# Kernel optimization log

Hardware: AMD Instinct MI355X
Metric: run time of the kernel (lower is better)

## Reference

```python
import jax, jax.numpy as jnp
import numpy as np

N_NODES = 50000
N_EDGES = 600000
IN_DIM = 128
HIDDEN = 128


def setup_inputs() -> dict:
    key = jax.random.key(0)
    k1, k2, k3, k4 = jax.random.split(key, 4)
    x = jax.random.normal(k1, (N_NODES, IN_DIM), dtype=jnp.float32)
    edge_index = jax.random.randint(k2, (2, N_EDGES), 0, N_NODES, dtype=jnp.int64)
    # Glorot-ish init for the two GCN layer weights
    W1 = jax.random.normal(k3, (IN_DIM, HIDDEN), dtype=jnp.float32) / np.sqrt(IN_DIM)
    b1 = jnp.zeros((HIDDEN,), dtype=jnp.float32)
    W2 = jax.random.normal(k4, (HIDDEN, HIDDEN), dtype=jnp.float32) / np.sqrt(HIDDEN)
    b2 = jnp.zeros((HIDDEN,), dtype=jnp.float32)
    return {"x": x, "edge_index": edge_index, "W1": W1, "b1": b1, "W2": W2, "b2": b2}


def _gcn_layer(x, W, b, src, dst, deg_inv_sqrt, n_nodes):
    # GCNConv: out = D^{-1/2} (A + I) D^{-1/2} X W + b, computed edge-wise.
    xw = x @ W                                           # [N, H] dense GEMM
    norm = deg_inv_sqrt[src] * deg_inv_sqrt[dst]         # [E+N]
    msg = xw[src] * norm[:, None]                        # gather + scale, [E+N, H]
    agg = jax.ops.segment_sum(msg, dst, num_segments=n_nodes)  # scatter-add
    return agg + b


def reference(x, edge_index, W1, b1, W2, b2):
    n_nodes = x.shape[0]
    loop = jnp.arange(n_nodes, dtype=edge_index.dtype)
    # add self-loops once; shared by both layers (same graph)
    src = jnp.concatenate([edge_index[0], loop])
    dst = jnp.concatenate([edge_index[1], loop])
    deg = jax.ops.segment_sum(jnp.ones_like(src, dtype=x.dtype), dst, num_segments=n_nodes)
    deg_inv_sqrt = jnp.where(deg > 0, jax.lax.rsqrt(jnp.maximum(deg, 1.0)), 0.0)

    h = jax.nn.relu(_gcn_layer(x, W1, b1, src, dst, deg_inv_sqrt, n_nodes))
    h = jax.nn.relu(_gcn_layer(h, W2, b2, src, dst, deg_inv_sqrt, n_nodes))
    return h
```

## Files before the change

kernel.cpp:

```cpp
#include <hip/hip_runtime.h>
#include <hip/hip_bf16.h>

#define DIM 128
#define CHUNK 4096
#define CAP 4096
typedef __hip_bfloat16 bf16;
typedef __attribute__((ext_vector_type(8))) short bf16x8;
typedef __attribute__((ext_vector_type(4))) float f32x4;

__global__ void prep_kernel(int* __restrict__ bcursor, int nbuck,
                            const int* __restrict__ ei, int E, int* __restrict__ misc,
                            const float* __restrict__ W1, const float* __restrict__ W2,
                            bf16* __restrict__ Wsw1, bf16* __restrict__ Wsw2) {
    if (blockIdx.x == 0) {
        for (int i = threadIdx.x; i < nbuck; i += 256) bcursor[i] = i * CAP;
    } else if (blockIdx.x == 1) {
        __shared__ int s_or;
        if (threadIdx.x == 0) s_or = 0;
        __syncthreads();
        int lim = E < 16384 ? E : 16384;
        int acc = 0;
        for (int j = threadIdx.x; j < lim; j += 256) acc |= ei[2 * j + 1];
        if (acc) atomicOr(&s_or, 1);
        __syncthreads();
        if (threadIdx.x == 0) misc[1] = s_or;
    } else {
        int id = (blockIdx.x - 2) * 256 + threadIdx.x;
        const float* W = (id < 2048) ? W1 : W2;
        bf16* Wsw = (id < 2048) ? Wsw1 : Wsw2;
        int t = id & 2047;
        int f = t >> 6, l = t & 63;
        int kt = f >> 3, nt = f & 7;
        int q = l >> 4, m = l & 15;
        bf16 tmp[8];
        #pragma unroll
        for (int j = 0; j < 8; ++j)
            tmp[j] = __float2bfloat16(W[(size_t)(kt * 32 + q * 8 + j) * DIM + nt * 16 + m]);
        *(bf16x8*)(Wsw + (size_t)t * 8) = *(const bf16x8*)tmp;
    }
}

template <bool XF32>
__device__ __forceinline__ void gemm_body(const void* __restrict__ Xv,
                                          const bf16* __restrict__ Wsw,
                                          bf16* __restrict__ Y, int N,
                                          int gw, int nw, int lane,
                                          float* sld) {
    int m = lane & 15, q = lane >> 4;
    const bf16x8* bp = (const bf16x8*)Wsw;
    for (int t = gw; t * 16 + 16 <= N; t += nw) {
        int base = t * 16;
        bf16x8 a[4];
        if (XF32) {
            const float* xp = (const float*)Xv + (size_t)(base + m) * DIM + q * 8;
            #pragma unroll
            for (int kt = 0; kt < 4; ++kt) {
                float4 v0 = *(const float4*)(xp + kt * 32);
                float4 v1 = *(const float4*)(xp + kt * 32 + 4);
                bf16 tt[8] = {__float2bfloat16(v0.x), __float2bfloat16(v0.y),
                              __float2bfloat16(v0.z), __float2bfloat16(v0.w),
                              __float2bfloat16(v1.x), __float2bfloat16(v1.y),
                              __float2bfloat16(v1.z), __float2bfloat16(v1.w)};
                a[kt] = *(const bf16x8*)tt;
            }
        } else {
            const bf16* xp = (const bf16*)Xv + (size_t)(base + m) * DIM + q * 8;
            #pragma unroll
            for (int kt = 0; kt < 4; ++kt)
                a[kt] = *(const bf16x8*)(xp + kt * 32);
        }
        f32x4 acc[8];
        #pragma unroll
        for (int nt = 0; nt < 8; ++nt) acc[nt] = (f32x4){0.f, 0.f, 0.f, 0.f};
        #pragma unroll
        for (int kt = 0; kt < 4; ++kt) {
            #pragma unroll
            for (int nt = 0; nt < 8; ++nt) {
                bf16x8 bfr = bp[(size_t)(kt * 8 + nt) * 64 + lane];
                acc[nt] = __builtin_amdgcn_mfma_f32_16x16x32_bf16(a[kt], bfr, acc[nt], 0, 0, 0);
            }
        }
        #pragma unroll
        for (int nt = 0; nt < 8; ++nt)
            #pragma unroll
            for (int r = 0; r < 4; ++r)
                sld[(q * 4 + r) * 132 + nt * 16 + m] = acc[nt][r];
        asm volatile("s_waitcnt lgkmcnt(0)" ::: "memory");
        #pragma unroll
        for (int i = 0; i < 4; ++i) {
            int row = i * 4 + q;
            const float* rp = sld + row * 132 + m * 8;
            float4 v0 = *(const float4*)rp;
            float4 v1 = *(const float4*)(rp + 4);
            alignas(16) bf16 tt[8] = {
                __float2bfloat16(v0.x), __float2bfloat16(v0.y),
                __float2bfloat16(v0.z), __float2bfloat16(v0.w),
                __float2bfloat16(v1.x), __float2bfloat16(v1.y),
                __float2bfloat16(v1.z), __float2bfloat16(v1.w)};
            *(uint4*)(Y + (size_t)(base + row) * DIM + m * 8) = *(const uint4*)tt;
        }
        asm volatile("s_waitcnt lgkmcnt(0)" ::: "memory");
    }
}

__global__ __launch_bounds__(256)
void scatter_gemm1(const int* __restrict__ ei, int E, const int* __restrict__ misc,
                   int* __restrict__ bcursor, unsigned* __restrict__ staged,
                   int nbuck, int nchunks,
                   const float* __restrict__ X, const bf16* __restrict__ Wsw,
                   bf16* __restrict__ Y, int N) {
    __shared__ float smem[4][16 * 132];
    int bx = blockIdx.x;
    if (bx < nchunks) {
        int* s_cnt  = (int*)&smem[0][0];
        int* s_base = s_cnt + 512;
        int* s_fill = s_cnt + 1024;
        for (int i = threadIdx.x; i < nbuck; i += 256) { s_cnt[i] = 0; s_fill[i] = 0; }
        __syncthreads();
        int flagI = misc[1];
        int c0 = bx * CHUNK;
        int cn = min(E - c0, CHUNK);
        for (int i = threadIdx.x; i < cn; i += 256) {
            int e = c0 + i;
            int d = (flagI == 0) ? ei[2 * E + 2 * e] : ei[E + e];
            atomicAdd(&s_cnt[d >> 7], 1);
        }
        __syncthreads();
        for (int i = threadIdx.x; i < nbuck; i += 256) {
            int c = s_cnt[i];
            s_base[i] = c ? atomicAdd(&bcursor[i], c) : 0;
        }
        __syncthreads();
        for (int i = threadIdx.x; i < cn; i += 256) {
            int e = c0 + i;
            int s, d;
            if (flagI == 0) { s = ei[2 * e]; d = ei[2 * E + 2 * e]; }
            else            { s = ei[e];     d = ei[E + e]; }
            int b = d >> 7;
            int r = s_base[b] + atomicAdd(&s_fill[b], 1);
            if (r < (b + 1) * CAP)
                staged[r] = ((unsigned)s << 7) | (unsigned)(d & 127);
        }
    } else {
        int wid = threadIdx.x >> 6, lane = threadIdx.x & 63;
        int ngw = (gridDim.x - nchunks) * 4;
        gemm_body<true>(X, Wsw, Y, N, (bx - nchunks) * 4 + wid, ngw, lane, smem[wid]);
    }
}

__global__ void bucket_sort(const unsigned* __restrict__ staged,
                            const int* __restrict__ bcursor,
                            int* __restrict__ csr, int* __restrict__ rowstart,
                            int* __restrict__ cnt, float* __restrict__ dis, int N) {
    __shared__ int s_cnt[128], s_off[128], s_fill[128], s_scan[128];
    int b = blockIdx.x, tid = threadIdx.x;
    int seg0 = b * CAP;
    int n = min(bcursor[b] - seg0, CAP);
    if (tid < 128) { s_cnt[tid] = 0; s_fill[tid] = 0; }
    __syncthreads();
    for (int i = tid; i < n; i += 256)
        atomicAdd(&s_cnt[staged[seg0 + i] & 127u], 1);
    __syncthreads();
    int v = (tid < 128) ? s_cnt[tid] : 0;
    if (tid < 128) s_scan[tid] = v;
    __syncthreads();
    for (int off = 1; off < 128; off <<= 1) {
        int t = (tid < 128 && tid >= off) ? s_scan[tid - off] : 0;
        __syncthreads();
        if (tid < 128) s_scan[tid] += t;
        __syncthreads();
    }
    if (tid < 128) {
        s_off[tid] = s_scan[tid] - v;
        int node = b * 128 + tid;
        if (node < N) {
            cnt[node] = v;
            rowstart[node] = seg0 + s_off[tid];
            dis[node] = rsqrtf((float)(v + 1));
        }
    }
    __syncthreads();
    for (int i = tid; i < n; i += 256) {
        unsigned p = staged[seg0 + i];
        int dl = p & 127u;
        int r = atomicAdd(&s_fill[dl], 1);
        csr[seg0 + s_off[dl] + r] = (int)(p >> 7);
    }
}

__device__ __forceinline__ void fma8(float* a, uint4 v, float ds) {
    a[0] = fmaf(__uint_as_float(v.x << 16), ds, a[0]);
    a[1] = fmaf(__uint_as_float(v.x & 0xffff0000u), ds, a[1]);
    a[2] = fmaf(__uint_as_float(v.y << 16), ds, a[2]);
    a[3] = fmaf(__uint_as_float(v.y & 0xffff0000u), ds, a[3]);
    a[4] = fmaf(__uint_as_float(v.z << 16), ds, a[4]);
    a[5] = fmaf(__uint_as_float(v.z & 0xffff0000u), ds, a[5]);
    a[6] = fmaf(__uint_as_float(v.w << 16), ds, a[6]);
    a[7] = fmaf(__uint_as_float(v.w & 0xffff0000u), ds, a[7]);
}

__device__ __forceinline__ void add8(float* a, uint4 v) {
    a[0] += __uint_as_float(v.x << 16);
    a[1] += __uint_as_float(v.x & 0xffff0000u);
    a[2] += __uint_as_float(v.y << 16);
    a[3] += __uint_as_float(v.y & 0xffff0000u);
    a[4] += __uint_as_float(v.z << 16);
    a[5] += __uint_as_float(v.z & 0xffff0000u);
    a[6] += __uint_as_float(v.w << 16);
    a[7] += __uint_as_float(v.w & 0xffff0000u);
}

__global__ __launch_bounds__(256, 4)
void agg1_gemm2(const uint4* __restrict__ Y, const int* __restrict__ rowstart,
                const int* __restrict__ cnt, const int* __restrict__ csr,
                const float* __restrict__ dis, const float* __restrict__ bias,
                const bf16* __restrict__ Wsw, bf16* __restrict__ Y2, int N) {
    __shared__ __align__(16) bf16 h_lds[16][136];
    __shared__ float s_out[16 * 132];
    int wave = threadIdx.x >> 6, lane = threadIdx.x & 63;
    int sub = lane >> 4, cl = lane & 15;
    int base = blockIdx.x * 16;
    int node = base + wave * 4 + sub;
    bool alive = node < N;

    float acc[4][8];
    #pragma unroll
    for (int j = 0; j < 4; ++j)
        #pragma unroll
        for (int k = 0; k < 8; ++k) acc[j][k] = 0.f;

    float dn = 0.f;
    if (alive) {
        int e0 = rowstart[node], e1 = e0 + cnt[node];
        dn = dis[node];
        fma8(acc[3], Y[(size_t)node * 16 + cl], dn);

        int e = e0;
        while (e + 8 <= e1) {
            int s[8];
            #pragma unroll
            for (int j = 0; j < 8; ++j) s[j] = csr[e + j];
            uint4 v[8]; float dv[8];
            #pragma unroll
            for (int j = 0; j < 8; ++j) { v[j] = Y[(size_t)s[j] * 16 + cl]; dv[j] = dis[s[j]]; }
            #pragma unroll
            for (int j = 0; j < 8; ++j) fma8(acc[j & 3], v[j], dv[j]);
            e += 8;
        }
        if (e + 4 <= e1) {
            int s[4];
            #pragma unroll
            for (int j = 0; j < 4; ++j) s[j] = csr[e + j];
            uint4 v[4]; float dv[4];
            #pragma unroll
            for (int j = 0; j < 4; ++j) { v[j] = Y[(size_t)s[j] * 16 + cl]; dv[j] = dis[s[j]]; }
            #pragma unroll
            for (int j = 0; j < 4; ++j) fma8(acc[j], v[j], dv[j]);
            e += 4;
        }
        for (; e < e1; ++e) {
            int s = csr[e];
            fma8(acc[0], Y[(size_t)s * 16 + cl], dis[s]);
        }
    }
    {
        float s8[8];
        #pragma unroll
        for (int k = 0; k < 8; ++k)
            s8[k] = (acc[0][k] + acc[1][k]) + (acc[2][k] + acc[3][k]);
        float4 b0 = ((const float4*)bias)[2 * cl];
        float4 b1 = ((const float4*)bias)[2 * cl + 1];
        alignas(16) bf16 t[8];
        t[0] = __float2bfloat16(alive ? fmaxf(dn * s8[0] + b0.x, 0.f) : 0.f);
        t[1] = __float2bfloat16(alive ? fmaxf(dn * s8[1] + b0.y, 0.f) : 0.f);
        t[2] = __float2bfloat16(alive ? fmaxf(dn * s8[2] + b0.z, 0.f) : 0.f);
        t[3] = __float2bfloat16(alive ? fmaxf(dn * s8[3] + b0.w, 0.f) : 0.f);
        t[4] = __float2bfloat16(alive ? fmaxf(dn * s8[4] + b1.x, 0.f) : 0.f);
        t[5] = __float2bfloat16(alive ? fmaxf(dn * s8[5] + b1.y, 0.f) : 0.f);
        t[6] = __float2bfloat16(alive ? fmaxf(dn * s8[6] + b1.z, 0.f) : 0.f);
        t[7] = __float2bfloat16(alive ? fmaxf(dn * s8[7] + b1.w, 0.f) : 0.f);
        *(uint4*)&h_lds[wave * 4 + sub][cl * 8] = *(const uint4*)t;
    }
    __syncthreads();

    int m = cl, q = sub;
    bf16x8 a[4];
    #pragma unroll
    for (int kt = 0; kt < 4; ++kt)
        a[kt] = *(const bf16x8*)&h_lds[m][q * 8 + kt * 32];
    const bf16x8* bp = (const bf16x8*)Wsw;
    f32x4 g[2];
    g[0] = (f32x4){0.f, 0.f, 0.f, 0.f};
    g[1] = (f32x4){0.f, 0.f, 0.f, 0.f};
    #pragma unroll
    for (int kt = 0; kt < 4; ++kt) {
        #pragma unroll
        for (int j = 0; j < 2; ++j) {
            int nt = wave * 2 + j;
            bf16x8 bfr = bp[(size_t)(kt * 8 + nt) * 64 + lane];
            g[j] = __builtin_amdgcn_mfma_f32_16x16x32_bf16(a[kt], bfr, g[j], 0, 0, 0);
        }
    }
    #pragma unroll
    for (int j = 0; j < 2; ++j)
        #pragma unroll
        for (int r = 0; r < 4; ++r)
            s_out[(q * 4 + r) * 132 + (wave * 2 + j) * 16 + m] = g[j][r];
    __syncthreads();

    int on = threadIdx.x >> 4;
    int oc = (threadIdx.x & 15) * 8;
    if (base + on < N) {
        float ds = dis[base + on];
        const float* rp = s_out + on * 132 + oc;
        float4 v0 = *(const float4*)rp;
        float4 v1 = *(const float4*)(rp + 4);
        alignas(16) bf16 t[8] = {
            __float2bfloat16(v0.x * ds), __float2bfloat16(v0.y * ds),
            __float2bfloat16(v0.z * ds), __float2bfloat16(v0.w * ds),
            __float2bfloat16(v1.x * ds), __float2bfloat16(v1.y * ds),
            __float2bfloat16(v1.z * ds), __float2bfloat16(v1.w * ds)};
        *(uint4*)(Y2 + (size_t)(base + on) * DIM + oc) = *(const uint4*)t;
    }
}

__global__ __launch_bounds__(256, 4)
void aggregate_final(const uint4* __restrict__ Y, const int* __restrict__ rowstart,
                     const int* __restrict__ cnt, const int* __restrict__ csr,
                     const float* __restrict__ dis, const float* __restrict__ bias,
                     float4* __restrict__ Of, int N) {
    int wave = threadIdx.x >> 6;
    int lane = threadIdx.x & 63;
    int sub = lane >> 4, cl = lane & 15;
    int node = blockIdx.x * 16 + wave * 4 + sub;
    if (node >= N) return;
    int e0 = rowstart[node], e1 = e0 + cnt[node];

    float acc[4][8];
    #pragma unroll
    for (int j = 0; j < 4; ++j)
        #pragma unroll
        for (int k = 0; k < 8; ++k) acc[j][k] = 0.f;

    float dn = dis[node];
    add8(acc[3], Y[(size_t)node * 16 + cl]);

    int e = e0;
    while (e + 8 <= e1) {
        int s[8];
        #pragma unroll
        for (int j = 0; j < 8; ++j) s[j] = csr[e + j];
        uint4 v[8];
        #pragma unroll
        for (int j = 0; j < 8; ++j) v[j] = Y[(size_t)s[j] * 16 + cl];
        #pragma unroll
        for (int j = 0; j < 8; ++j) add8(acc[j & 3], v[j]);
        e += 8;
    }
    if (e + 4 <= e1) {
        int s[4];
        #pragma unroll
        for (int j = 0; j < 4; ++j) s[j] = csr[e + j];
        uint4 v[4];
        #pragma unroll
        for (int j = 0; j < 4; ++j) v[j] = Y[(size_t)s[j] * 16 + cl];
        #pragma unroll
        for (int j = 0; j < 4; ++j) add8(acc[j], v[j]);
        e += 4;
    }
    for (; e < e1; ++e)
        add8(acc[0], Y[(size_t)csr[e] * 16 + cl]);

    float s8[8];
    #pragma unroll
    for (int k = 0; k < 8; ++k)
        s8[k] = (acc[0][k] + acc[1][k]) + (acc[2][k] + acc[3][k]);

    float4 b0 = ((const float4*)bias)[2 * cl];
    float4 b1 = ((const float4*)bias)[2 * cl + 1];
    float o[8];
    o[0] = fmaxf(dn * s8[0] + b0.x, 0.f);
    o[1] = fmaxf(dn * s8[1] + b0.y, 0.f);
    o[2] = fmaxf(dn * s8[2] + b0.z, 0.f);
    o[3] = fmaxf(dn * s8[3] + b0.w, 0.f);
    o[4] = fmaxf(dn * s8[4] + b1.x, 0.f);
    o[5] = fmaxf(dn * s8[5] + b1.y, 0.f);
    o[6] = fmaxf(dn * s8[6] + b1.z, 0.f);
    o[7] = fmaxf(dn * s8[7] + b1.w, 0.f);
    Of[(size_t)node * 32 + 2 * cl]     = make_float4(o[0], o[1], o[2], o[3]);
    Of[(size_t)node * 32 + 2 * cl + 1] = make_float4(o[4], o[5], o[6], o[7]);
}

extern "C" void kernel_launch(void* const* d_in, const int* in_sizes, int n_in,
                              void* d_out, int out_size, void* d_ws, size_t ws_size,
                              hipStream_t stream) {
    const float* x  = (const float*)d_in[0];
    const int*   ei = (const int*)d_in[1];
    const float* W1 = (const float*)d_in[2];
    const float* b1 = (const float*)d_in[3];
    const float* W2 = (const float*)d_in[4];
    const float* b2 = (const float*)d_in[5];

    int N = in_sizes[0] / DIM;
    int E = in_sizes[1] / 2;
    int nbuck = (N + 127) / 128;
    int nchunks = (E + CHUNK - 1) / CHUNK;

    char* w = (char*)d_ws;
    size_t used = 0;
    auto carve = [&](size_t bytes) {
        char* p = w + used;
        used += (bytes + 255) & ~(size_t)255;
        return p;
    };
    int*      misc     = (int*)     carve(256);
    int*      bcursor  = (int*)     carve((size_t)(nbuck + 1) * 4);
    unsigned* staged   = (unsigned*)carve((size_t)nbuck * CAP * 4);
    int*      csr      = (int*)     carve((size_t)nbuck * CAP * 4);
    int*      rowstart = (int*)     carve((size_t)N * 4);
    int*      cnt      = (int*)     carve((size_t)N * 4);
    float*    dis      = (float*)   carve((size_t)N * 4);
    bf16*     ybuf     = (bf16*)    carve((size_t)N * DIM * 2);
    bf16*     hbuf     = (bf16*)    carve((size_t)N * DIM * 2);
    bf16*     Wsw1     = (bf16*)    carve((size_t)DIM * DIM * 2);
    bf16*     Wsw2     = (bf16*)    carve((size_t)DIM * DIM * 2);

    prep_kernel <<<18, 256, 0, stream>>>(bcursor, nbuck, ei, E, misc, W1, W2, Wsw1, Wsw2);
    scatter_gemm1<<<nchunks + 784, 256, 0, stream>>>(ei, E, misc, bcursor, staged,
                                                     nbuck, nchunks, x, Wsw1, ybuf, N);
    bucket_sort <<<nbuck, 256, 0, stream>>>(staged, bcursor, csr, rowstart, cnt, dis, N);

    int ablocks = (N + 15) / 16;
    agg1_gemm2<<<ablocks, 256, 0, stream>>>((const uint4*)ybuf, rowstart, cnt, csr,
                                            dis, b1, Wsw2, hbuf, N);
    aggregate_final<<<ablocks, 256, 0, stream>>>((const uint4*)hbuf, rowstart, cnt, csr,
                                                 dis, b2, (float4*)d_out, N);
}
```

Baseline: 181.8 us.

## Precompute degrees, fold source normalization into GEMM1, fuse bucket sort with layer-1 aggregation

Node degrees are now counted up front with global atomics, in new detect_zero, prep2 and dis_k kernels. The result lets the first GEMM scale its output rows by D^{-1/2} of the source node. Layer-1 aggregation then becomes a plain sum with no per-edge dis gather. The bucket sort kernel is fused with layer-1 aggregation and the second GEMM into one 512-thread block per 128-node bucket, which removes a launch and a round trip of csr/cnt/dis through global memory. The trade-offs are two extra small launches, an extra atomic pass over all edges, and far fewer blocks (one per bucket) for the latency-bound gather phase, which may hurt latency hiding.

```diff
diff --git a/kernel.cpp b/kernel.cpp
--- a/kernel.cpp
+++ b/kernel.cpp
@@ -8,13 +8,9 @@
 typedef __attribute__((ext_vector_type(8))) short bf16x8;
 typedef __attribute__((ext_vector_type(4))) float f32x4;
 
-__global__ void prep_kernel(int* __restrict__ bcursor, int nbuck,
-                            const int* __restrict__ ei, int E, int* __restrict__ misc,
-                            const float* __restrict__ W1, const float* __restrict__ W2,
-                            bf16* __restrict__ Wsw1, bf16* __restrict__ Wsw2) {
+__global__ void detect_zero(const int* __restrict__ ei, int E, int* __restrict__ misc,
+                            int* __restrict__ cnt, int N) {
     if (blockIdx.x == 0) {
-        for (int i = threadIdx.x; i < nbuck; i += 256) bcursor[i] = i * CAP;
-    } else if (blockIdx.x == 1) {
         __shared__ int s_or;
         if (threadIdx.x == 0) s_or = 0;
         __syncthreads();
@@ -25,7 +21,21 @@
         __syncthreads();
         if (threadIdx.x == 0) misc[1] = s_or;
     } else {
-        int id = (blockIdx.x - 2) * 256 + threadIdx.x;
+        int i = (blockIdx.x - 1) * 256 + threadIdx.x;
+        if (i < N) cnt[i] = 0;
+    }
+}
+
+__global__ void prep2(int* __restrict__ bcursor, int nbuck,
+                      const int* __restrict__ ei, int E, const int* __restrict__ misc,
+                      const float* __restrict__ W1, const float* __restrict__ W2,
+                      bf16* __restrict__ Wsw1, bf16* __restrict__ Wsw2,
+                      int* __restrict__ cnt) {
+    int bx = blockIdx.x;
+    if (bx == 0) {
+        for (int i = threadIdx.x; i < nbuck; i += 256) bcursor[i] = i * CAP;
+    } else if (bx <= 16) {
+        int id = (bx - 1) * 256 + threadIdx.x;
         const float* W = (id < 2048) ? W1 : W2;
         bf16* Wsw = (id < 2048) ? Wsw1 : Wsw2;
         int t = id & 2047;
@@ -37,12 +47,24 @@
         for (int j = 0; j < 8; ++j)
             tmp[j] = __float2bfloat16(W[(size_t)(kt * 32 + q * 8 + j) * DIM + nt * 16 + m]);
         *(bf16x8*)(Wsw + (size_t)t * 8) = *(const bf16x8*)tmp;
-    }
-}
-
-template <bool XF32>
-__device__ __forceinline__ void gemm_body(const void* __restrict__ Xv,
+    } else {
+        int flagI = misc[1];
+        int g0 = (bx - 17) * 256 + threadIdx.x;
+        for (int e = g0; e < E; e += 64 * 256) {
+            int d = (flagI == 0) ? ei[2 * E + 2 * e] : ei[E + e];
+            atomicAdd(&cnt[d], 1);
+        }
+    }
+}
+
+__global__ void dis_k(const int* __restrict__ cnt, float* __restrict__ dis, int N) {
+    int i = blockIdx.x * 256 + threadIdx.x;
+    if (i < N) dis[i] = rsqrtf((float)(cnt[i] + 1));
+}
+
+__device__ __forceinline__ void gemm_body(const float* __restrict__ Xv,
                                           const bf16* __restrict__ Wsw,
+                                          const float* __restrict__ disv,
                                           bf16* __restrict__ Y, int N,
                                           int gw, int nw, int lane,
                                           float* sld) {
@@ -51,23 +73,16 @@
     for (int t = gw; t * 16 + 16 <= N; t += nw) {
         int base = t * 16;
         bf16x8 a[4];
-        if (XF32) {
-            const float* xp = (const float*)Xv + (size_t)(base + m) * DIM + q * 8;
-            #pragma unroll
-            for (int kt = 0; kt < 4; ++kt) {
-                float4 v0 = *(const float4*)(xp + kt * 32);
-                float4 v1 = *(const float4*)(xp + kt * 32 + 4);
-                bf16 tt[8] = {__float2bfloat16(v0.x), __float2bfloat16(v0.y),
-                              __float2bfloat16(v0.z), __float2bfloat16(v0.w),
-                              __float2bfloat16(v1.x), __float2bfloat16(v1.y),
-                              __float2bfloat16(v1.z), __float2bfloat16(v1.w)};
-                a[kt] = *(const bf16x8*)tt;
-            }
-        } else {
-            const bf16* xp = (const bf16*)Xv + (size_t)(base + m) * DIM + q * 8;
-            #pragma unroll
-            for (int kt = 0; kt < 4; ++kt)
-                a[kt] = *(const bf16x8*)(xp + kt * 32);
+        const float* xp = Xv + (size_t)(base + m) * DIM + q * 8;
+        #pragma unroll
+        for (int kt = 0; kt < 4; ++kt) {
+            float4 v0 = *(const float4*)(xp + kt * 32);
+            float4 v1 = *(const float4*)(xp + kt * 32 + 4);
+            bf16 tt[8] = {__float2bfloat16(v0.x), __float2bfloat16(v0.y),
+                          __float2bfloat16(v0.z), __float2bfloat16(v0.w),
+                          __float2bfloat16(v1.x), __float2bfloat16(v1.y),
+                          __float2bfloat16(v1.z), __float2bfloat16(v1.w)};
+            a[kt] = *(const bf16x8*)tt;
         }
         f32x4 acc[8];
         #pragma unroll
@@ -89,14 +104,15 @@
         #pragma unroll
         for (int i = 0; i < 4; ++i) {
             int row = i * 4 + q;
+            float ds = disv[base + row];
             const float* rp = sld + row * 132 + m * 8;
             float4 v0 = *(const float4*)rp;
             float4 v1 = *(const float4*)(rp + 4);
             alignas(16) bf16 tt[8] = {
-                __float2bfloat16(v0.x), __float2bfloat16(v0.y),
-                __float2bfloat16(v0.z), __float2bfloat16(v0.w),
-                __float2bfloat16(v1.x), __float2bfloat16(v1.y),
-                __float2bfloat16(v1.z), __float2bfloat16(v1.w)};
+                __float2bfloat16(v0.x * ds), __float2bfloat16(v0.y * ds),
+                __float2bfloat16(v0.z * ds), __float2bfloat16(v0.w * ds),
+                __float2bfloat16(v1.x * ds), __float2bfloat16(v1.y * ds),
+                __float2bfloat16(v1.z * ds), __float2bfloat16(v1.w * ds)};
             *(uint4*)(Y + (size_t)(base + row) * DIM + m * 8) = *(const uint4*)tt;
         }
         asm volatile("s_waitcnt lgkmcnt(0)" ::: "memory");
@@ -108,7 +124,7 @@
                    int* __restrict__ bcursor, unsigned* __restrict__ staged,
                    int nbuck, int nchunks,
                    const float* __restrict__ X, const bf16* __restrict__ Wsw,
-                   bf16* __restrict__ Y, int N) {
+                   const float* __restrict__ dis, bf16* __restrict__ Y, int N) {
     __shared__ float smem[4][16 * 132];
     int bx = blockIdx.x;
     if (bx < nchunks) {
@@ -144,59 +160,8 @@
     } else {
         int wid = threadIdx.x >> 6, lane = threadIdx.x & 63;
         int ngw = (gridDim.x - nchunks) * 4;
-        gemm_body<true>(X, Wsw, Y, N, (bx - nchunks) * 4 + wid, ngw, lane, smem[wid]);
-    }
-}
-
-__global__ void bucket_sort(const unsigned* __restrict__ staged,
-                            const int* __restrict__ bcursor,
-                            int* __restrict__ csr, int* __restrict__ rowstart,
-                            int* __restrict__ cnt, float* __restrict__ dis, int N) {
-    __shared__ int s_cnt[128], s_off[128], s_fill[128], s_scan[128];
-    int b = blockIdx.x, tid = threadIdx.x;
-    int seg0 = b * CAP;
-    int n = min(bcursor[b] - seg0, CAP);
-    if (tid < 128) { s_cnt[tid] = 0; s_fill[tid] = 0; }
-    __syncthreads();
-    for (int i = tid; i < n; i += 256)
-        atomicAdd(&s_cnt[staged[seg0 + i] & 127u], 1);
-    __syncthreads();
-    int v = (tid < 128) ? s_cnt[tid] : 0;
-    if (tid < 128) s_scan[tid] = v;
-    __syncthreads();
-    for (int off = 1; off < 128; off <<= 1) {
-        int t = (tid < 128 && tid >= off) ? s_scan[tid - off] : 0;
-        __syncthreads();
-        if (tid < 128) s_scan[tid] += t;
-        __syncthreads();
-    }
-    if (tid < 128) {
-        s_off[tid] = s_scan[tid] - v;
-        int node = b * 128 + tid;
-        if (node < N) {
-            cnt[node] = v;
-            rowstart[node] = seg0 + s_off[tid];
-            dis[node] = rsqrtf((float)(v + 1));
-        }
-    }
-    __syncthreads();
-    for (int i = tid; i < n; i += 256) {
-        unsigned p = staged[seg0 + i];
-        int dl = p & 127u;
-        int r = atomicAdd(&s_fill[dl], 1);
-        csr[seg0 + s_off[dl] + r] = (int)(p >> 7);
-    }
-}
-
-__device__ __forceinline__ void fma8(float* a, uint4 v, float ds) {
-    a[0] = fmaf(__uint_as_float(v.x << 16), ds, a[0]);
-    a[1] = fmaf(__uint_as_float(v.x & 0xffff0000u), ds, a[1]);
-    a[2] = fmaf(__uint_as_float(v.y << 16), ds, a[2]);
-    a[3] = fmaf(__uint_as_float(v.y & 0xffff0000u), ds, a[3]);
-    a[4] = fmaf(__uint_as_float(v.z << 16), ds, a[4]);
-    a[5] = fmaf(__uint_as_float(v.z & 0xffff0000u), ds, a[5]);
-    a[6] = fmaf(__uint_as_float(v.w << 16), ds, a[6]);
-    a[7] = fmaf(__uint_as_float(v.w & 0xffff0000u), ds, a[7]);
+        gemm_body(X, Wsw, dis, Y, N, (bx - nchunks) * 4 + wid, ngw, lane, smem[wid]);
+    }
 }
 
 __device__ __forceinline__ void add8(float* a, uint4 v) {
@@ -210,117 +175,154 @@
     a[7] += __uint_as_float(v.w & 0xffff0000u);
 }
 
-__global__ __launch_bounds__(256, 4)
-void agg1_gemm2(const uint4* __restrict__ Y, const int* __restrict__ rowstart,
-                const int* __restrict__ cnt, const int* __restrict__ csr,
-                const float* __restrict__ dis, const float* __restrict__ bias,
-                const bf16* __restrict__ Wsw, bf16* __restrict__ Y2, int N) {
-    __shared__ __align__(16) bf16 h_lds[16][136];
-    __shared__ float s_out[16 * 132];
-    int wave = threadIdx.x >> 6, lane = threadIdx.x & 63;
-    int sub = lane >> 4, cl = lane & 15;
-    int base = blockIdx.x * 16;
-    int node = base + wave * 4 + sub;
-    bool alive = node < N;
-
-    float acc[4][8];
-    #pragma unroll
-    for (int j = 0; j < 4; ++j)
-        #pragma unroll
-        for (int k = 0; k < 8; ++k) acc[j][k] = 0.f;
-
-    float dn = 0.f;
-    if (alive) {
-        int e0 = rowstart[node], e1 = e0 + cnt[node];
-        dn = dis[node];
-        fma8(acc[3], Y[(size_t)node * 16 + cl], dn);
-
-        int e = e0;
-        while (e + 8 <= e1) {
-            int s[8];
+__device__ __forceinline__ void row_accum(float acc[4][8], const uint4* __restrict__ Y,
+                                          const int* __restrict__ csr,
+                                          int e0, int e1, int cl) {
+    int e = e0;
+    while (e + 8 <= e1) {
+        int s[8];
+        #pragma unroll
+        for (int j = 0; j < 8; ++j) s[j] = csr[e + j];
+        uint4 v[8];
+        #pragma unroll
+        for (int j = 0; j < 8; ++j) v[j] = Y[(size_t)s[j] * 16 + cl];
+        #pragma unroll
+        for (int j = 0; j < 8; ++j) add8(acc[j & 3], v[j]);
+        e += 8;
+    }
+    if (e + 4 <= e1) {
+        int s[4];
+        #pragma unroll
+        for (int j = 0; j < 4; ++j) s[j] = csr[e + j];
+        uint4 v[4];
+        #pragma unroll
+        for (int j = 0; j < 4; ++j) v[j] = Y[(size_t)s[j] * 16 + cl];
+        #pragma unroll
+        for (int j = 0; j < 4; ++j) add8(acc[j], v[j]);
+        e += 4;
+    }
+    for (; e < e1; ++e)
+        add8(acc[0], Y[(size_t)csr[e] * 16 + cl]);
+}
+
+__global__ __launch_bounds__(512, 4)
+void sort_agg1_gemm2(const uint4* __restrict__ Y, const unsigned* __restrict__ staged,
+                     const int* __restrict__ bcursor, int* __restrict__ csr,
+                     int* __restrict__ rowstart, const float* __restrict__ bias,
+                     const bf16* __restrict__ Wsw, bf16* __restrict__ Y2, int N) {
+    __shared__ int s_cnt[128], s_off[128], s_fill[128], s_scan[128];
+    __shared__ __align__(16) float big[8 * 16 * 132];
+    bf16* hT = (bf16*)big;
+    int tid = threadIdx.x;
+    int b = blockIdx.x;
+    int seg0 = b * CAP, base = b * 128;
+    int n = min(bcursor[b] - seg0, CAP);
+
+    if (tid < 128) { s_cnt[tid] = 0; s_fill[tid] = 0; }
+    __syncthreads();
+    for (int i = tid; i < n; i += 512)
+        atomicAdd(&s_cnt[staged[seg0 + i] & 127u], 1);
+    __syncthreads();
+    int v = (tid < 128) ? s_cnt[tid] : 0;
+    if (tid < 128) s_scan[tid] = v;
+    __syncthreads();
+    for (int off = 1; off < 128; off <<= 1) {
+        int t = (tid < 128 && tid >= off) ? s_scan[tid - off] : 0;
+        __syncthreads();
+        if (tid < 128) s_scan[tid] += t;
+        __syncthreads();
+    }
+    if (tid < 128) {
+        s_off[tid] = s_scan[tid] - v;
+        int node = base + tid;
+        if (node < N) rowstart[node] = seg0 + s_off[tid];
+    }
+    __syncthreads();
+    for (int i = tid; i < n; i += 512) {
+        unsigned p = staged[seg0 + i];
+        int dl = p & 127u;
+        int r = atomicAdd(&s_fill[dl], 1);
+        csr[seg0 + s_off[dl] + r] = (int)(p >> 7);
+    }
+    __threadfence_block();
+    __syncthreads();
+
+    #pragma unroll
+    for (int r4 = 0; r4 < 4; ++r4) {
+        int lrow = r4 * 32 + (tid >> 4);
+        int cl = tid & 15;
+        int node = base + lrow;
+        bool alive = node < N;
+        float acc[4][8];
+        #pragma unroll
+        for (int j = 0; j < 4; ++j)
             #pragma unroll
-            for (int j = 0; j < 8; ++j) s[j] = csr[e + j];
-            uint4 v[8]; float dv[8];
-            #pragma unroll
-            for (int j = 0; j < 8; ++j) { v[j] = Y[(size_t)s[j] * 16 + cl]; dv[j] = dis[s[j]]; }
-            #pragma unroll
-            for (int j = 0; j < 8; ++j) fma8(acc[j & 3], v[j], dv[j]);
-            e += 8;
-        }
-        if (e + 4 <= e1) {
-            int s[4];
-            #pragma unroll
-            for (int j = 0; j < 4; ++j) s[j] = csr[e + j];
-            uint4 v[4]; float dv[4];
-            #pragma unroll
-            for (int j = 0; j < 4; ++j) { v[j] = Y[(size_t)s[j] * 16 + cl]; dv[j] = dis[s[j]]; }
-            #pragma unroll
-            for (int j = 0; j < 4; ++j) fma8(acc[j], v[j], dv[j]);
-            e += 4;
-        }
-        for (; e < e1; ++e) {
-            int s = csr[e];
-            fma8(acc[0], Y[(size_t)s * 16 + cl], dis[s]);
-        }
-    }
-    {
+            for (int k = 0; k < 8; ++k) acc[j][k] = 0.f;
+        float dn = 0.f;
+        if (alive) {
+            dn = rsqrtf((float)(s_cnt[lrow] + 1));
+            add8(acc[3], Y[(size_t)node * 16 + cl]);
+            int e0 = seg0 + s_off[lrow];
+            row_accum(acc, Y, csr, e0, e0 + s_cnt[lrow], cl);
+        }
         float s8[8];
         #pragma unroll
         for (int k = 0; k < 8; ++k)
             s8[k] = (acc[0][k] + acc[1][k]) + (acc[2][k] + acc[3][k]);
         float4 b0 = ((const float4*)bias)[2 * cl];
         float4 b1 = ((const float4*)bias)[2 * cl + 1];
-        alignas(16) bf16 t[8];
-        t[0] = __float2bfloat16(alive ? fmaxf(dn * s8[0] + b0.x, 0.f) : 0.f);
-        t[1] = __float2bfloat16(alive ? fmaxf(dn * s8[1] + b0.y, 0.f) : 0.f);
-        t[2] = __float2bfloat16(alive ? fmaxf(dn * s8[2] + b0.z, 0.f) : 0.f);
-        t[3] = __float2bfloat16(alive ? fmaxf(dn * s8[3] + b0.w, 0.f) : 0.f);
-        t[4] = __float2bfloat16(alive ? fmaxf(dn * s8[4] + b1.x, 0.f) : 0.f);
-        t[5] = __float2bfloat16(alive ? fmaxf(dn * s8[5] + b1.y, 0.f) : 0.f);
-        t[6] = __float2bfloat16(alive ? fmaxf(dn * s8[6] + b1.z, 0.f) : 0.f);
-        t[7] = __float2bfloat16(alive ? fmaxf(dn * s8[7] + b1.w, 0.f) : 0.f);
-        *(uint4*)&h_lds[wave * 4 + sub][cl * 8] = *(const uint4*)t;
-    }
-    __syncthreads();
-
-    int m = cl, q = sub;
+        float bb[8] = {b0.x, b0.y, b0.z, b0.w, b1.x, b1.y, b1.z, b1.w};
+        alignas(16) bf16 hh[8];
+        #pragma unroll
+        for (int j = 0; j < 8; ++j)
+            hh[j] = __float2bfloat16(alive ? fmaxf(dn * s8[j] + bb[j], 0.f) : 0.f);
+        *(uint4*)&hT[(size_t)lrow * 136 + cl * 8] = *(const uint4*)hh;
+    }
+    __syncthreads();
+
+    int wave = tid >> 6, lane = tid & 63;
+    int m = lane & 15, q = lane >> 4;
     bf16x8 a[4];
     #pragma unroll
     for (int kt = 0; kt < 4; ++kt)
-        a[kt] = *(const bf16x8*)&h_lds[m][q * 8 + kt * 32];
+        a[kt] = *(const bf16x8*)&hT[(size_t)(wave * 16 + m) * 136 + q * 8 + kt * 32];
+    __syncthreads();
+
     const bf16x8* bp = (const bf16x8*)Wsw;
-    f32x4 g[2];
-    g[0] = (f32x4){0.f, 0.f, 0.f, 0.f};
-    g[1] = (f32x4){0.f, 0.f, 0.f, 0.f};
-    #pragma unroll
-    for (int kt = 0; kt < 4; ++kt) {
-        #pragma unroll
-        for (int j = 0; j < 2; ++j) {
-            int nt = wave * 2 + j;
+    f32x4 acc[8];
+    #pragma unroll
+    for (int nt = 0; nt < 8; ++nt) acc[nt] = (f32x4){0.f, 0.f, 0.f, 0.f};
+    #pragma unroll
+    for (int kt = 0; kt < 4; ++kt)
+        #pragma unroll
+        for (int nt = 0; nt < 8; ++nt) {
             bf16x8 bfr = bp[(size_t)(kt * 8 + nt) * 64 + lane];
-            g[j] = __builtin_amdgcn_mfma_f32_16x16x32_bf16(a[kt], bfr, g[j], 0, 0, 0);
-        }
-    }
-    #pragma unroll
-    for (int j = 0; j < 2; ++j)
+            acc[nt] = __builtin_amdgcn_mfma_f32_16x16x32_bf16(a[kt], bfr, acc[nt], 0, 0, 0);
+        }
+    float* s_out = big + wave * (16 * 132);
+    #pragma unroll
+    for (int nt = 0; nt < 8; ++nt)
         #pragma unroll
         for (int r = 0; r < 4; ++r)
-            s_out[(q * 4 + r) * 132 + (wave * 2 + j) * 16 + m] = g[j][r];
-    __syncthreads();
-
-    int on = threadIdx.x >> 4;
-    int oc = (threadIdx.x & 15) * 8;
-    if (base + on < N) {
-        float ds = dis[base + on];
-        const float* rp = s_out + on * 132 + oc;
-        float4 v0 = *(const float4*)rp;
-        float4 v1 = *(const float4*)(rp + 4);
-        alignas(16) bf16 t[8] = {
-            __float2bfloat16(v0.x * ds), __float2bfloat16(v0.y * ds),
-            __float2bfloat16(v0.z * ds), __float2bfloat16(v0.w * ds),
-            __float2bfloat16(v1.x * ds), __float2bfloat16(v1.y * ds),
-            __float2bfloat16(v1.z * ds), __float2bfloat16(v1.w * ds)};
-        *(uint4*)(Y2 + (size_t)(base + on) * DIM + oc) = *(const uint4*)t;
+            s_out[(q * 4 + r) * 132 + nt * 16 + m] = acc[nt][r];
+    asm volatile("s_waitcnt lgkmcnt(0)" ::: "memory");
+    #pragma unroll
+    for (int i = 0; i < 4; ++i) {
+        int row = i * 4 + q;
+        int lrow = wave * 16 + row;
+        int node = base + lrow;
+        if (node < N) {
+            float ds = rsqrtf((float)(s_cnt[lrow] + 1));
+            const float* rp = s_out + row * 132 + m * 8;
+            float4 v0 = *(const float4*)rp;
+            float4 v1 = *(const float4*)(rp + 4);
+            alignas(16) bf16 tt[8] = {
+                __float2bfloat16(v0.x * ds), __float2bfloat16(v0.y * ds),
+                __float2bfloat16(v0.z * ds), __float2bfloat16(v0.w * ds),
+                __float2bfloat16(v1.x * ds), __float2bfloat16(v1.y * ds),
+                __float2bfloat16(v1.z * ds), __float2bfloat16(v1.w * ds)};
+            *(uint4*)(Y2 + (size_t)node * DIM + m * 8) = *(const uint4*)tt;
+        }
     }
 }
 
@@ -344,32 +346,7 @@
 
     float dn = dis[node];
     add8(acc[3], Y[(size_t)node * 16 + cl]);
-
-    int e = e0;
-    while (e + 8 <= e1) {
-        int s[8];
-        #pragma unroll
-        for (int j = 0; j < 8; ++j) s[j] = csr[e + j];
-        uint4 v[8];
-        #pragma unroll
-        for (int j = 0; j < 8; ++j) v[j] = Y[(size_t)s[j] * 16 + cl];
-        #pragma unroll
-        for (int j = 0; j < 8; ++j) add8(acc[j & 3], v[j]);
-        e += 8;
-    }
-    if (e + 4 <= e1) {
-        int s[4];
-        #pragma unroll
-        for (int j = 0; j < 4; ++j) s[j] = csr[e + j];
-        uint4 v[4];
-        #pragma unroll
-        for (int j = 0; j < 4; ++j) v[j] = Y[(size_t)s[j] * 16 + cl];
-        #pragma unroll
-        for (int j = 0; j < 4; ++j) add8(acc[j], v[j]);
-        e += 4;
-    }
-    for (; e < e1; ++e)
-        add8(acc[0], Y[(size_t)csr[e] * 16 + cl]);
+    row_accum(acc, Y, csr, e0, e1, cl);
 
     float s8[8];
     #pragma unroll
@@ -425,14 +402,15 @@
     bf16*     Wsw1     = (bf16*)    carve((size_t)DIM * DIM * 2);
     bf16*     Wsw2     = (bf16*)    carve((size_t)DIM * DIM * 2);
 
-    prep_kernel <<<18, 256, 0, stream>>>(bcursor, nbuck, ei, E, misc, W1, W2, Wsw1, Wsw2);
+    int zblocks = (N + 255) / 256;
+    detect_zero<<<1 + zblocks, 256, 0, stream>>>(ei, E, misc, cnt, N);
+    prep2<<<81, 256, 0, stream>>>(bcursor, nbuck, ei, E, misc, W1, W2, Wsw1, Wsw2, cnt);
+    dis_k<<<zblocks, 256, 0, stream>>>(cnt, dis, N);
     scatter_gemm1<<<nchunks + 784, 256, 0, stream>>>(ei, E, misc, bcursor, staged,
-                                                     nbuck, nchunks, x, Wsw1, ybuf, N);
-    bucket_sort <<<nbuck, 256, 0, stream>>>(staged, bcursor, csr, rowstart, cnt, dis, N);
-
+                                                     nbuck, nchunks, x, Wsw1, dis, ybuf, N);
+    sort_agg1_gemm2<<<nbuck, 512, 0, stream>>>((const uint4*)ybuf, staged, bcursor,
+                                               csr, rowstart, b1, Wsw2, hbuf, N);
     int ablocks = (N + 15) / 16;
-    agg1_gemm2<<<ablocks, 256, 0, stream>>>((const uint4*)ybuf, rowstart, cnt, csr,
-                                            dis, b1, Wsw2, hbuf, N);
     aggregate_final<<<ablocks, 256, 0, stream>>>((const uint4*)hbuf, rowstart, cnt, csr,
                                                  dis, b2, (float4*)d_out, N);
 }
```

After: 211.3 us. 16.3% more time.
